# Optimization experiments

Hardware: AMD Instinct MI355X
Metric: run time of the kernel (lower is better)

The kernel has to match this reference:

```python
import jax, jax.numpy as jnp
import numpy as np

N_HASHES = 4
CHUNK = 144


def conv2d(x, w, b, pad):
    y = jax.lax.conv_general_dilated(x, w, (1, 1), [(pad, pad), (pad, pad)],
                                     dimension_numbers=('NCHW', 'OIHW', 'NCHW'))
    return y + b[None, :, None, None]


def resblock(x, w1, b1, w2, b2, ws=None, bs=None):
    # conv3x3 -> ReLU -> conv3x3 + skip (1x1 projection when channels change)
    h = conv2d(x, w1, b1, 1)
    h = jax.nn.relu(h)
    h = conv2d(h, w2, b2, 1)
    skip = x if ws is None else conv2d(x, ws, bs, 0)
    return skip + h


def _forward(feature_dec1, feature_dec2, reference_feature,
             mw1, mb1, mw2, mb2, mws, mbs,
             a1w1, a1b1, a1w2, a1b2, a2w1, a2b1, a2w2, a2b2,
             random_index):
    fd1 = jax.lax.stop_gradient(feature_dec1)  # is_detach=True default
    fd2 = jax.lax.stop_gradient(feature_dec2)
    B, C0, H, W = fd1.shape
    L = H * W
    # embeddings: (B, L, C) with C = C0 // reduction, and (B, L, C0) assemblies
    f1 = resblock(fd1, mw1, mb1, mw2, mb2, mws, mbs).reshape(B, -1, L).transpose(0, 2, 1)
    f2 = resblock(fd2, mw1, mb1, mw2, mb2, mws, mbs).reshape(B, -1, L).transpose(0, 2, 1)
    aux1 = resblock(fd1, a1w1, a1b1, a1w2, a1b2).reshape(B, -1, L).transpose(0, 2, 1)
    refe = resblock(reference_feature, a2w1, a2b1, a2w2, a2b2).reshape(B, -1, L).transpose(0, 2, 1)
    C = f1.shape[-1]
    inv_random_index = jnp.argsort(random_index)
    hb = min(2 * L // CHUNK + (2 * L // CHUNK) % 2, 128)
    f1f2 = jnp.concatenate([f1, f2], axis=1)            # (B, 2L, C)
    # LSH hashing (random rotations drawn with a fixed key, matching randn-per-call in torch)
    rot = jax.random.normal(jax.random.key(42), (C, N_HASHES, hb // 2), dtype=f1f2.dtype)
    rv = jnp.einsum('btf,fhi->bhti', f1f2, rot)
    rv = jnp.concatenate([rv, -rv], axis=-1)
    codes = jnp.argmax(rv, axis=-1)                     # (B, nh, 2L)
    codes = codes + (jnp.arange(N_HASHES) * hb)[None, :, None]
    codes = codes[:, :, random_index].reshape(B, -1)    # (B, nh*2L)
    indices = jnp.argsort(codes, axis=-1)
    undo_sort = jnp.argsort(indices, axis=-1)
    mod_indices = (indices % 2) * L                     # faithful to torch `indices % 2 * L` precedence
    zo = jnp.concatenate([jnp.full((B, L), 0.01, f1.dtype),
                          jnp.full((B, L), 0.99, f1.dtype)], axis=1)
    f1f2_p = f1f2[:, random_index, :]
    q = jnp.take_along_axis(f1f2_p, mod_indices[:, :, None], axis=1)
    zo_p = zo[:, random_index]
    z = jnp.take_along_axis(zo_p, mod_indices, axis=1)
    refw = jnp.concatenate([aux1, refe], axis=1)[:, random_index, :]
    r = jnp.take_along_axis(refw, mod_indices[:, :, None], axis=1)
    rem = (2 * L) % CHUNK
    padding = CHUNK - rem if rem != 0 else 0
    qb = q.reshape(B, N_HASHES, 2 * L, C)
    zb = z.reshape(B, N_HASHES, 2 * L)
    rb = r.reshape(B, N_HASHES, 2 * L, -1)
    if padding:
        qb = jnp.concatenate([qb, qb[:, :, -padding:]], axis=2)
        zb = jnp.concatenate([zb, zb[:, :, -padding:]], axis=2)
        rb = jnp.concatenate([rb, rb[:, :, -padding:]], axis=2)
    k = qb.shape[2] // CHUNK
    qb = qb.reshape(B, N_HASHES, k, CHUNK, C)
    zb = zb.reshape(B, N_HASHES, k, CHUNK)
    rb = rb.reshape(B, N_HASHES, k, CHUNK, -1)
    # F.normalize(p=2, dim=-1, eps=5e-5)
    norm = jnp.sqrt(jnp.sum(qb * qb, axis=-1, keepdims=True))
    km = qb / jnp.maximum(norm, 5e-5)
    adj = lambda x: jnp.concatenate([x, jnp.roll(x, 1, axis=2), jnp.roll(x, -1, axis=2)], axis=3)
    km, zb3, rb3 = adj(km), adj(zb), adj(rb)            # keys/vals over 3 adjacent buckets
    raw = jnp.einsum('bhkie,bhkje->bhkij', qb, km)      # (B,nh,k,144,432)
    w = jnp.exp(raw) * zb3[:, :, :, None, :]
    denom = jnp.sum(w, axis=-1, keepdims=True)
    score = w / denom
    bucket_score = denom.reshape(B, N_HASHES, -1)
    ret = jnp.einsum('bhkij,bhkje->bhkie', score, rb3)  # (B,nh,k,144,C0)
    CR = rb3.shape[-1]
    ret = ret.reshape(B, N_HASHES, -1, CR)
    if padding:
        ret = ret[:, :, :-padding]
        bucket_score = bucket_score[:, :, :-padding]
    ret = ret.reshape(B, N_HASHES * 2 * L, CR)
    bucket_score = bucket_score.reshape(B, -1)
    ret = jnp.take_along_axis(ret, undo_sort[:, :, None], axis=1)
    bucket_score = jnp.take_along_axis(bucket_score, undo_sort, axis=1)
    ret = ret.reshape(B, N_HASHES, 2 * L, CR)
    bucket_score = bucket_score.reshape(B, N_HASHES, 2 * L, 1)
    probs = bucket_score / jnp.sum(bucket_score, axis=1, keepdims=True)
    ret = jnp.sum(ret * probs, axis=1)                  # (B, 2L, CR)
    ret = ret.transpose(0, 2, 1)[:, :, inv_random_index]
    return ret.reshape(B, CR, 2, H, W)[:, :, 0]         # (B, C0, H, W)


def setup_inputs() -> dict:
    key = jax.random.key(0)
    ks = jax.random.split(key, 12)
    B, C0, H, W = 2, 64, 100, 100
    red = 4
    Cm = C0 // red
    s = jnp.float32(0.05)
    rn = lambda i, shape: jax.random.normal(ks[i], shape, dtype=jnp.float32)
    return {
        'feature_dec1': rn(0, (B, C0, H, W)),
        'feature_dec2': rn(1, (B, C0, H, W)),
        'reference_feature': rn(2, (B, C0, H, W)),
        'random_index': jax.random.permutation(ks[3], 2 * H * W).astype(jnp.int32),
        'mw1': rn(4, (Cm, C0, 3, 3)) * s, 'mb1': jnp.zeros((Cm,), jnp.float32),
        'mw2': rn(5, (Cm, Cm, 3, 3)) * s, 'mb2': jnp.zeros((Cm,), jnp.float32),
        'mws': rn(6, (Cm, C0, 1, 1)) * s, 'mbs': jnp.zeros((Cm,), jnp.float32),
        'a1w1': rn(7, (C0, C0, 3, 3)) * s, 'a1b1': jnp.zeros((C0,), jnp.float32),
        'a1w2': rn(8, (C0, C0, 3, 3)) * s, 'a1b2': jnp.zeros((C0,), jnp.float32),
        'a2w1': rn(9, (C0, C0, 3, 3)) * s, 'a2b1': jnp.zeros((C0,), jnp.float32),
        'a2w2': rn(10, (C0, C0, 3, 3)) * s, 'a2b2': jnp.zeros((C0,), jnp.float32),
    }


def reference(feature_dec1, feature_dec2, reference_feature, random_index,
              mw1, mb1, mw2, mb2, mws, mbs,
              a1w1, a1b1, a1w2, a1b2, a2w1, a2b1, a2w2, a2b2):
    return _forward(feature_dec1, feature_dec2, reference_feature,
                    mw1, mb1, mw2, mb2, mws, mbs,
                    a1w1, a1b1, a1w2, a1b2, a2w1, a2b1, a2w2, a2b2,
                    random_index)
```

## Files before the change

kernel.cpp:

```cpp
#include <hip/hip_runtime.h>

#define JAX_THREEFRY_PARTITIONABLE 1

namespace {

constexpr int BN   = 2;
constexpr int C0   = 64;
constexpr int HH   = 100;
constexpr int WWW  = 100;
constexpr int LL   = 10000;
constexpr int TL   = 20000;
constexpr int CHK  = 144;
constexpr int NCHK = 139;
constexpr int NPAD = 16;
constexpr int WINR = 432;

constexpr int OFF_ROT  = 0;
constexpr int OFF_WT1  = OFF_ROT + 4096;
constexpr int OFF_WT2  = OFF_WT1 + 9216;
constexpr int OFF_WTS  = OFF_WT2 + 2304;
constexpr int OFF_HT0  = OFF_WTS + 1024;
constexpr int OFF_HT1  = OFF_HT0 + 640000;
constexpr int OFF_HT2  = OFF_HT1 + 640000;
constexpr int OFF_HT3  = OFF_HT2 + 640000;
constexpr int OFF_F    = OFF_HT3 + 640000;
constexpr int OFF_SC   = OFF_F + 640000;
constexpr int OFF_CODE = OFF_SC + 272;
constexpr int OFF_RANK = OFF_CODE + 40000;
constexpr int OFF_N0   = OFF_RANK + 160000;
constexpr int OFF_INV  = OFF_N0 + 1112;
constexpr int OFF_AUX  = OFF_INV + 10000;

constexpr int AUXW = 36864;

__device__ __forceinline__ unsigned rotl32(unsigned v, int r) {
  return (v << r) | (v >> (32 - r));
}

__device__ void tf2x32(unsigned k0, unsigned k1, unsigned x0, unsigned x1,
                       unsigned& o0, unsigned& o1) {
  unsigned ks2 = k0 ^ k1 ^ 0x1BD11BDAu;
  x0 += k0; x1 += k1;
#define TFR(r) { x0 += x1; x1 = rotl32(x1, r); x1 ^= x0; }
  TFR(13) TFR(15) TFR(26) TFR(6)  x0 += k1;  x1 += ks2 + 1u;
  TFR(17) TFR(29) TFR(16) TFR(24) x0 += ks2; x1 += k0 + 2u;
  TFR(13) TFR(15) TFR(26) TFR(6)  x0 += k0;  x1 += k1 + 3u;
  TFR(17) TFR(29) TFR(16) TFR(24) x0 += k1;  x1 += ks2 + 4u;
  TFR(13) TFR(15) TFR(26) TFR(6)  x0 += ks2; x1 += k0 + 5u;
#undef TFR
  o0 = x0; o1 = x1;
}

__device__ float xla_erfinv(float x) {
#pragma clang fp contract(off)
  float w = -log1pf(-x * x);
  float p;
  if (w < 5.0f) {
    w = w - 2.5f;
    p = 2.81022636e-08f;
    p = 3.43273939e-07f  + p * w;
    p = -3.5233877e-06f  + p * w;
    p = -4.39150654e-06f + p * w;
    p = 0.00021858087f   + p * w;
    p = -0.00125372503f  + p * w;
    p = -0.00417768164f  + p * w;
    p = 0.246640727f     + p * w;
    p = 1.50140941f      + p * w;
  } else {
    w = sqrtf(w) - 3.0f;
    p = -0.000200214257f;
    p = 0.000100950558f + p * w;
    p = 0.00134934322f  + p * w;
    p = -0.00367342844f + p * w;
    p = 0.00573950773f  + p * w;
    p = -0.0076224613f  + p * w;
    p = 0.00943887047f  + p * w;
    p = 1.00167406f     + p * w;
    p = 2.83297682f     + p * w;
  }
  return p * x;
}

__global__ void k_prep(const float* __restrict__ mw1, const float* __restrict__ mw2,
                       const float* __restrict__ mws,
                       const float* __restrict__ a1w1, const float* __restrict__ a1w2,
                       const float* __restrict__ a2w1, const float* __restrict__ a2w2,
                       const int* __restrict__ ri,
                       float* __restrict__ rotT, float* __restrict__ wT1,
                       float* __restrict__ wT2, float* __restrict__ wTs,
                       float* __restrict__ auxT, int* __restrict__ inv) {
  int gid = blockIdx.x * 256 + threadIdx.x;
  if (gid < 4 * AUXW) {
    int wsel = gid / AUXW, j = gid % AUXW;
    const float* src = (wsel == 0) ? a1w1 : (wsel == 1) ? a1w2 : (wsel == 2) ? a2w1 : a2w2;
    int co = j / 576, r = j % 576;
    auxT[wsel * AUXW + r * 64 + co] = src[j];
    return;
  }
  int g2 = gid - 4 * AUXW;
  if (g2 < 4096) {
    int i = g2;
    unsigned o0, o1, bits;
#if JAX_THREEFRY_PARTITIONABLE
    tf2x32(0u, 42u, 0u, (unsigned)i, o0, o1);
    bits = o0 ^ o1;
#else
    if (i < 2048) { tf2x32(0u, 42u, (unsigned)i, (unsigned)(i + 2048), o0, o1); bits = o0; }
    else          { tf2x32(0u, 42u, (unsigned)(i - 2048), (unsigned)i, o0, o1); bits = o1; }
#endif
    unsigned fb = (bits >> 9) | 0x3f800000u;
    float f = __uint_as_float(fb) - 1.0f;
    const float lo = __uint_as_float(0xBF7FFFFFu);
    float u = fmaxf(lo, f * 2.0f + lo);
    float r = __uint_as_float(0x3FB504F3u) * xla_erfinv(u);
    int c = i >> 8, h = (i >> 6) & 3, j = i & 63;
    rotT[(h * 64 + j) * 16 + c] = r;
    return;
  }
  int g3 = g2 - 4096;
  if (g3 < 9216) {
    { int o = g3 / 576; int r = g3 % 576; wT1[r * 16 + o] = mw1[g3]; }
    if (g3 < 2304) { int o = g3 / 144; int r = g3 % 144; wT2[r * 16 + o] = mw2[g3]; }
    if (g3 < 1024) { int o = g3 / 64;  int ci = g3 % 64; wTs[ci * 16 + o] = mws[g3]; }
    return;
  }
  int g4 = g3 - 9216;
  if (g4 < TL) {
    int p = ri[g4];
    if (p < LL) inv[p] = g4;
  }
}

__global__ __launch_bounds__(256) void k_conv1(
    const float* __restrict__ fd1, const float* __restrict__ fd2,
    const float* __restrict__ wT1,
    float* __restrict__ ht0, float* __restrict__ ht1,
    float* __restrict__ ht2, float* __restrict__ ht3) {
  int x = blockIdx.x;
  int blk = (x & 7) * 98 + (x >> 3);
  int kq = blk & 3;
  int rest = blk >> 2;
  int n = rest / 49, tile = rest % 49;
  int ty0 = (tile / 7) * 16, tx0 = (tile % 7) * 16;
  const float* in = ((n >> 1) ? fd2 : fd1) + (n & 1) * (C0 * LL) + (kq * 16) * LL;
  float* htk = ((kq == 0) ? ht0 : (kq == 1) ? ht1 : (kq == 2) ? ht2 : ht3) + n * 16 * LL;
  int tid = threadIdx.x;
  int co = tid & 15, yl = tid >> 4;

  __shared__ float sIn[16 * 18 * 20];
  __shared__ float sW[144 * 16];

  for (int i = tid; i < 144 * 16; i += 256) sW[i] = wT1[kq * 2304 + i];
  for (int idx = tid; idx < 16 * 18 * 18; idx += 256) {
    int ci = idx / 324, r = idx % 324, iy = r / 18, ix = r % 18;
    int gy = ty0 - 1 + iy, gx = tx0 - 1 + ix;
    float v = 0.f;
    if (gy >= 0 && gy < HH && gx >= 0 && gx < WWW) v = in[ci * LL + gy * WWW + gx];
    sIn[ci * 360 + iy * 20 + ix] = v;
  }
  __syncthreads();

  float acc[16];
#pragma unroll
  for (int p = 0; p < 16; ++p) acc[p] = 0.f;

  for (int cc = 0; cc < 4; ++cc) {
    float w[4][9];
#pragma unroll
    for (int c4 = 0; c4 < 4; ++c4)
#pragma unroll
      for (int t = 0; t < 9; ++t)
        w[c4][t] = sW[((cc * 4 + c4) * 9 + t) * 16 + co];
#pragma unroll
    for (int c4 = 0; c4 < 4; ++c4) {
      const float* rowb = &sIn[(cc * 4 + c4) * 360 + yl * 20];
#pragma unroll
      for (int dy = 0; dy < 3; ++dy) {
        const float* r = rowb + dy * 20;
        float v[18];
#pragma unroll
        for (int k = 0; k < 18; ++k) v[k] = r[k];
#pragma unroll
        for (int dx = 0; dx < 3; ++dx) {
          float wv = w[c4][dy * 3 + dx];
#pragma unroll
          for (int p = 0; p < 16; ++p) acc[p] = fmaf(v[p + dx], wv, acc[p]);
        }
      }
    }
  }

  int yv = ty0 + yl;
  if (yv < HH) {
    float* op = htk + co * LL + yv * WWW;
#pragma unroll
    for (int g = 0; g < 4; ++g) {
      int xg = tx0 + g * 4;
      if (xg < WWW) {
        float4 s = make_float4(acc[g * 4], acc[g * 4 + 1], acc[g * 4 + 2], acc[g * 4 + 3]);
        *(float4*)&op[xg] = s;
      }
    }
  }
}

__global__ __launch_bounds__(512) void k_conv2(
    const float* __restrict__ fd1, const float* __restrict__ fd2,
    const float* __restrict__ ht0, const float* __restrict__ ht1,
    const float* __restrict__ ht2, const float* __restrict__ ht3,
    const float* __restrict__ wT2, const float* __restrict__ mb1,
    const float* __restrict__ mb2, const float* __restrict__ wTs,
    const float* __restrict__ mbs, float* __restrict__ F) {
  int xx = blockIdx.x;
  int xcd = xx & 7, slot = xx >> 3;
  int blk = (xcd < 4) ? (xcd * 46 + slot) : (184 + (xcd - 4) * 45 + slot);
  int n = blk / 91, tile = blk % 91;
  int yt = tile / 7, xt = tile % 7;
  int ty0 = yt * 8, tx0 = xt * 16;
  int src = n >> 1, b = n & 1;
  const float* in = (src ? fd2 : fd1) + b * (C0 * LL);
  const float* h0 = ht0 + n * 16 * LL;
  const float* h1 = ht1 + n * 16 * LL;
  const float* h2 = ht2 + n * 16 * LL;
  const float* h3 = ht3 + n * 16 * LL;
  int tid = threadIdx.x;
  int co = tid & 15, xq = (tid >> 4) & 3, yl = tid >> 6;

  __shared__ float sW2[144 * 16];
  __shared__ float sWs[64 * 16];
  __shared__ float sH[16 * 10 * 20];
  __shared__ float sSkip[16 * 8 * 17];

  for (int i = tid; i < 144 * 16; i += 512) sW2[i] = wT2[i];
  for (int i = tid; i < 64 * 16; i += 512) sWs[i] = wTs[i];
  for (int idx = tid; idx < 16 * 10 * 18; idx += 512) {
    int ci = idx / 180, r = idx % 180, iy = r / 18, ix = r % 18;
    int gy = ty0 - 1 + iy, gx = tx0 - 1 + ix;
    float v = 0.f;
    if (gy >= 0 && gy < HH && gx >= 0 && gx < WWW) {
      int o = ci * LL + gy * WWW + gx;
      v = fmaxf(h0[o] + h1[o] + h2[o] + h3[o] + mb1[ci], 0.f);
    }
    sH[ci * 200 + iy * 20 + ix] = v;
  }
  __syncthreads();

  float acc[4];
  float bias = mb2[co] + mbs[co];
#pragma unroll
  for (int p = 0; p < 4; ++p) acc[p] = bias;

  for (int ci = 0; ci < 16; ++ci) {
    const float* rowb = &sH[ci * 200 + yl * 20 + xq * 4];
#pragma unroll
    for (int dy = 0; dy < 3; ++dy) {
      const float* r = rowb + dy * 20;
      float v[6];
#pragma unroll
      for (int k = 0; k < 6; ++k) v[k] = r[k];
#pragma unroll
      for (int dx = 0; dx < 3; ++dx) {
        float wv = sW2[(ci * 9 + dy * 3 + dx) * 16 + co];
#pragma unroll
        for (int p = 0; p < 4; ++p) acc[p] = fmaf(v[p + dx], wv, acc[p]);
      }
    }
  }

  for (int cc = 0; cc < 4; ++cc) {
    __syncthreads();
    for (int idx = tid; idx < 16 * 8 * 16; idx += 512) {
      int ci = idx >> 7, r = idx & 127, iy = r >> 4, ix = r & 15;
      int gy = ty0 + iy, gx = tx0 + ix;
      float v = 0.f;
      if (gy < HH && gx < WWW) v = in[(cc * 16 + ci) * LL + gy * WWW + gx];
      sSkip[(ci * 8 + iy) * 17 + ix] = v;
    }
    __syncthreads();
    for (int c16 = 0; c16 < 16; ++c16) {
      float wv = sWs[(cc * 16 + c16) * 16 + co];
      const float* sv = &sSkip[(c16 * 8 + yl) * 17 + xq * 4];
#pragma unroll
      for (int p = 0; p < 4; ++p) acc[p] = fmaf(sv[p], wv, acc[p]);
    }
  }

  int yv = ty0 + yl;
  if (yv < HH) {
    float* Fb = F + (b * TL + src * LL + yv * WWW) * 16 + co;
#pragma unroll
    for (int p = 0; p < 4; ++p) {
      int xv = tx0 + xq * 4 + p;
      if (xv < WWW) Fb[xv * 16] = acc[p];
    }
  }
}

__global__ __launch_bounds__(256) void k_codes(
    const float* __restrict__ F, const float* __restrict__ rotT,
    const int* __restrict__ ri, unsigned char* __restrict__ codes) {
  int bh = blockIdx.y;
  int b = bh >> 2, h = bh & 3;
  __shared__ float srot[1024];
  int tid = threadIdx.x;
  for (int i = tid; i < 1024; i += 256) srot[i] = rotT[h * 1024 + i];
  __syncthreads();
  int t = blockIdx.x * 256 + tid;
  if (t >= TL) return;
  int pos = ri[t];
  const float* Fr = F + (b * TL + pos) * 16;
  float q[16];
#pragma unroll
  for (int c = 0; c < 16; ++c) q[c] = Fr[c];
  float best = -1e30f; int bi = 0;
  float worst = 1e30f; int wi = 0;
  for (int j = 0; j < 64; ++j) {
    float v = 0.f;
    const float* rp = srot + j * 16;
#pragma unroll
    for (int c = 0; c < 16; ++c) v = fmaf(q[c], rp[c], v);
    if (v > best)  { best = v;  bi = j; }
    if (v < worst) { worst = v; wi = j; }
  }
  int code = (best >= -worst) ? bi : (64 + wi);
  codes[bh * TL + t] = (unsigned char)code;
}

__global__ __launch_bounds__(256) void k_sort(
    const unsigned char* __restrict__ codes,
    int* __restrict__ rank_of, int* __restrict__ n0g) {
  int bh = blockIdx.x;
  const unsigned char* keys = codes + bh * TL;
  __shared__ unsigned short cnt[240][128];
  __shared__ unsigned int totals[128];
  __shared__ unsigned int baseoff[128];
  __shared__ unsigned int n0s[NCHK];
  int tid = threadIdx.x;
  for (int i = tid; i < 240 * 128 / 2; i += 256) ((unsigned int*)cnt)[i] = 0u;
  for (int i = tid; i < NCHK; i += 256) n0s[i] = 0u;
  __syncthreads();
  const int SEG = 84;
  int base = tid * SEG;
  int nloc = (tid < 240) ? (TL - base) : 0;
  if (nloc > SEG) nloc = SEG;
  if (nloc < 0) nloc = 0;
  for (int e = 0; e < nloc; ++e) cnt[tid][keys[base + e]]++;
  __syncthreads();
  if (tid < 128) {
    unsigned int s = 0;
    for (int g = 0; g < 240; ++g) s += cnt[g][tid];
    totals[tid] = s;
  }
  __syncthreads();
  if (tid == 0) {
    unsigned int run = 0;
    for (int c = 0; c < 128; ++c) { baseoff[c] = run; run += totals[c]; }
  }
  __syncthreads();
  if (tid < 128) {
    unsigned int run = baseoff[tid];
    for (int g = 0; g < 240; ++g) {
      unsigned int v = cnt[g][tid];
      cnt[g][tid] = (unsigned short)run;
      run += v;
    }
  }
  __syncthreads();
  for (int e = 0; e < nloc; ++e) {
    int idx = base + e;
    int c = keys[idx];
    int r = cnt[tid][c]++;
    rank_of[bh * TL + idx] = r;
    if (!(idx & 1)) {
      atomicAdd(&n0s[r / CHK], 1u);
      if (r >= TL - NPAD) atomicAdd(&n0s[NCHK - 1], 1u);
    }
  }
  __syncthreads();
  for (int i = tid; i < NCHK; i += 256) n0g[bh * NCHK + i] = (int)n0s[i];
}

__global__ __launch_bounds__(576) void k_point(
    const float* __restrict__ fd1, const float* __restrict__ refin,
    const int* __restrict__ ri, const float* __restrict__ auxT,
    const float* __restrict__ a1b1, const float* __restrict__ a1b2,
    const float* __restrict__ a2b1, const float* __restrict__ a2b2,
    const float* __restrict__ F, float* __restrict__ SC) {
  int tid = threadIdx.x;
  if (blockIdx.x == 4) {
#pragma clang fp contract(off)
    int b = tid;
    if (b >= BN) return;
    int j0 = ri[0], jL = ri[LL];
    const float* qA = F + (b * TL + j0) * 16;
    const float* qB = F + (b * TL + jL) * 16;
    float nA = 0.f, nB = 0.f;
    for (int c = 0; c < 16; ++c) { nA += qA[c] * qA[c]; nB += qB[c] * qB[c]; }
    float mA = fmaxf(sqrtf(nA), 5e-5f), mB = fmaxf(sqrtf(nB), 5e-5f);
    float d00 = 0.f, d01 = 0.f, d10 = 0.f, d11 = 0.f;
    for (int c = 0; c < 16; ++c) {
      float kAc = qA[c] / mA, kBc = qB[c] / mB;
      d00 += qA[c] * kAc; d01 += qA[c] * kBc;
      d10 += qB[c] * kAc; d11 += qB[c] * kBc;
    }
    float zA = (j0 < LL) ? 0.01f : 0.99f;
    float zB = (jL < LL) ? 0.01f : 0.99f;
    float* sc = SC + b * 136;
    sc[0] = expf(d00) * zA; sc[1] = expf(d01) * zB;
    sc[2] = expf(d10) * zA; sc[3] = expf(d11) * zB;
    return;
  }
  int b = blockIdx.x & 1, which = blockIdx.x >> 1;
  int pos = ri[which * LL];
  const float *in, *w1T, *b1, *w2T, *b2;
  int sp;
  if (pos < LL) {
    in = fd1 + b * C0 * LL; w1T = auxT; b1 = a1b1; w2T = auxT + AUXW; b2 = a1b2; sp = pos;
  } else {
    in = refin + b * C0 * LL; w1T = auxT + 2 * AUXW; b1 = a2b1; w2T = auxT + 3 * AUXW;
    b2 = a2b2; sp = pos - LL;
  }
  int y = sp / WWW, x = sp % WWW;

  __shared__ float sPatch[64][25];
  __shared__ float sW[144 * 64];
  __shared__ float sH[9][64];
  __shared__ float sPart[9][64];

  for (int idx = tid; idx < 64 * 25; idx += 576) {
    int ci = idx / 25, pp = idx % 25;
    int gy = y - 2 + pp / 5, gx = x - 2 + pp % 5;
    float v = 0.f;
    if (gy >= 0 && gy < HH && gx >= 0 && gx < WWW) v = in[ci * LL + gy * WWW + gx];
    sPatch[ci][pp] = v;
  }

  int p = tid / 64, ch = tid & 63;
  int p3 = p / 3, pm = p % 3;
  int yy = y + p3 - 1, xx = x + pm - 1;
  bool inb = (yy >= 0) && (yy < HH) && (xx >= 0) && (xx < WWW);

  float acc0 = 0.f, acc1 = 0.f;
  for (int cc = 0; cc < 4; ++cc) {
    __syncthreads();
    for (int i = tid; i < 144 * 64; i += 576) sW[i] = w1T[cc * 9216 + i];
    __syncthreads();
    if (inb) {
#pragma unroll
      for (int ci = 0; ci < 16; ++ci) {
        const float* wp = &sW[ci * 9 * 64 + ch];
        const float* pr = &sPatch[cc * 16 + ci][0];
#pragma unroll
        for (int t = 0; t < 9; ++t) {
          float v = pr[(p3 + t / 3) * 5 + (pm + t % 3)];
          if (ci & 1) acc1 = fmaf(v, wp[t * 64], acc1);
          else        acc0 = fmaf(v, wp[t * 64], acc0);
        }
      }
    }
  }
  sH[p][ch] = inb ? fmaxf(acc0 + acc1 + b1[ch], 0.f) : 0.f;
  __syncthreads();

  {
    float part = 0.f;
    const float* wbase = w2T + p * 64 + ch;
    for (int ci = 0; ci < 64; ++ci) part = fmaf(sH[p][ci], wbase[ci * 9 * 64], part);
    sPart[p][ch] = part;
  }
  __syncthreads();
  if (tid < 64) {
    int co = tid;
    float a = in[co * LL + y * WWW + x] + b2[co];
#pragma unroll
    for (int g = 0; g < 9; ++g) a += sPart[g][co];
    SC[b * 136 + 4 + which * 64 + co] = a;
  }
}

__global__ __launch_bounds__(256) void k_out(
    const int* __restrict__ inv, const int* __restrict__ rank_of,
    const int* __restrict__ n0, const float* __restrict__ SC,
    float* __restrict__ out) {
  int b = blockIdx.y;
  int p = blockIdx.x * 256 + threadIdx.x;
  if (p >= LL) return;
  int t = inv[p];
  int si = t & 1;
  float e0 = SC[b * 136 + si * 2 + 0];
  float e1 = SC[b * 136 + si * 2 + 1];
  float s0 = 0.f, s1 = 0.f;
  for (int h = 0; h < 4; ++h) {
    int r = rank_of[(b * 4 + h) * TL + t];
    int k = r / CHK;
    int km = (k == 0) ? NCHK - 1 : k - 1;
    int kp = (k == NCHK - 1) ? 0 : k + 1;
    const int* nb = n0 + (b * 4 + h) * NCHK;
    int W0 = nb[k] + nb[km] + nb[kp];
    s0 += (float)W0 * e0;
    s1 += (float)(WINR - W0) * e1;
  }
  float invd = 1.f / (s0 + s1);
  float al = s0 * invd;
  float be = s1 * invd;
  const float* rA = SC + b * 136 + 4;
  const float* rB = rA + 64;
  float* o = out + b * C0 * LL + p;
#pragma unroll
  for (int c = 0; c < 64; ++c) o[c * LL] = al * rA[c] + be * rB[c];
}

}

extern "C" void kernel_launch(void* const* d_in, const int* in_sizes, int n_in,
                              void* d_out, int out_size, void* d_ws, size_t ws_size,
                              hipStream_t stream) {
  const float* fd1  = (const float*)d_in[0];
  const float* fd2  = (const float*)d_in[1];
  const float* reff = (const float*)d_in[2];
  const int*   ri   = (const int*)d_in[3];
  const float* mw1  = (const float*)d_in[4];
  const float* mb1  = (const float*)d_in[5];
  const float* mw2  = (const float*)d_in[6];
  const float* mb2  = (const float*)d_in[7];
  const float* mws  = (const float*)d_in[8];
  const float* mbs  = (const float*)d_in[9];
  const float* a1w1 = (const float*)d_in[10];
  const float* a1b1 = (const float*)d_in[11];
  const float* a1w2 = (const float*)d_in[12];
  const float* a1b2 = (const float*)d_in[13];
  const float* a2w1 = (const float*)d_in[14];
  const float* a2b1 = (const float*)d_in[15];
  const float* a2w2 = (const float*)d_in[16];
  const float* a2b2 = (const float*)d_in[17];

  float* ws = (float*)d_ws;
  float* rotT = ws + OFF_ROT;
  float* wT1  = ws + OFF_WT1;
  float* wT2  = ws + OFF_WT2;
  float* wTs  = ws + OFF_WTS;
  float* ht0  = ws + OFF_HT0;
  float* ht1  = ws + OFF_HT1;
  float* ht2  = ws + OFF_HT2;
  float* ht3  = ws + OFF_HT3;
  float* F    = ws + OFF_F;
  float* SC   = ws + OFF_SC;
  unsigned char* codes = (unsigned char*)(ws + OFF_CODE);
  int* rank_of = (int*)(ws + OFF_RANK);
  int* n0      = (int*)(ws + OFF_N0);
  int* invp    = (int*)(ws + OFF_INV);
  float* auxT  = ws + OFF_AUX;

  k_prep<<<dim3(707), dim3(256), 0, stream>>>(mw1, mw2, mws, a1w1, a1w2, a2w1, a2w2,
                                              ri, rotT, wT1, wT2, wTs, auxT, invp);
  k_conv1<<<dim3(784), dim3(256), 0, stream>>>(fd1, fd2, wT1, ht0, ht1, ht2, ht3);
  k_conv2<<<dim3(364), dim3(512), 0, stream>>>(fd1, fd2, ht0, ht1, ht2, ht3, wT2,
                                               mb1, mb2, wTs, mbs, F);
  k_codes<<<dim3(79, 8), dim3(256), 0, stream>>>(F, rotT, ri, codes);
  k_sort<<<dim3(8), dim3(256), 0, stream>>>(codes, rank_of, n0);
  k_point<<<dim3(5), dim3(576), 0, stream>>>(fd1, reff, ri, auxT, a1b1, a1b2,
                                             a2b1, a2b2, F, SC);
  k_out<<<dim3(40, 2), dim3(256), 0, stream>>>(invp, rank_of, n0, SC, (float*)d_out);
}
```

Measured before the change: 132.8 us.

## Shrink conv1 tiles, fuse codes with point kernel, split output by channel

conv1 now uses 8-row tiles with 512 threads and 4 outputs per thread, giving more blocks and fewer registers per thread. The LSH code computation and the aux point evaluation are merged into one launch, which removes a kernel launch and lets the small point blocks overlap with hashing. k_out gains a z-dimension splitting its 64 output channels into 4 groups for more parallelism. Smaller conv tiles raise halo overhead and reload weights more often.

```diff
diff --git a/kernel.cpp b/kernel.cpp
--- a/kernel.cpp
+++ b/kernel.cpp
@@ -131,38 +131,39 @@
   }
 }
 
-__global__ __launch_bounds__(256) void k_conv1(
+__global__ __launch_bounds__(512) void k_conv1(
     const float* __restrict__ fd1, const float* __restrict__ fd2,
     const float* __restrict__ wT1,
     float* __restrict__ ht0, float* __restrict__ ht1,
     float* __restrict__ ht2, float* __restrict__ ht3) {
   int x = blockIdx.x;
-  int blk = (x & 7) * 98 + (x >> 3);
+  int blk = (x & 7) * 182 + (x >> 3);
   int kq = blk & 3;
   int rest = blk >> 2;
-  int n = rest / 49, tile = rest % 49;
-  int ty0 = (tile / 7) * 16, tx0 = (tile % 7) * 16;
+  int n = rest / 91, tile = rest % 91;
+  int yt = tile / 7, xt = tile % 7;
+  int ty0 = yt * 8, tx0 = xt * 16;
   const float* in = ((n >> 1) ? fd2 : fd1) + (n & 1) * (C0 * LL) + (kq * 16) * LL;
   float* htk = ((kq == 0) ? ht0 : (kq == 1) ? ht1 : (kq == 2) ? ht2 : ht3) + n * 16 * LL;
   int tid = threadIdx.x;
-  int co = tid & 15, yl = tid >> 4;
-
-  __shared__ float sIn[16 * 18 * 20];
+  int co = tid & 15, xq = (tid >> 4) & 3, yl = tid >> 6;
+
+  __shared__ float sIn[16 * 10 * 20];
   __shared__ float sW[144 * 16];
 
-  for (int i = tid; i < 144 * 16; i += 256) sW[i] = wT1[kq * 2304 + i];
-  for (int idx = tid; idx < 16 * 18 * 18; idx += 256) {
-    int ci = idx / 324, r = idx % 324, iy = r / 18, ix = r % 18;
+  for (int i = tid; i < 144 * 16; i += 512) sW[i] = wT1[kq * 2304 + i];
+  for (int idx = tid; idx < 16 * 10 * 18; idx += 512) {
+    int ci = idx / 180, r = idx % 180, iy = r / 18, ix = r % 18;
     int gy = ty0 - 1 + iy, gx = tx0 - 1 + ix;
     float v = 0.f;
     if (gy >= 0 && gy < HH && gx >= 0 && gx < WWW) v = in[ci * LL + gy * WWW + gx];
-    sIn[ci * 360 + iy * 20 + ix] = v;
-  }
-  __syncthreads();
-
-  float acc[16];
-#pragma unroll
-  for (int p = 0; p < 16; ++p) acc[p] = 0.f;
+    sIn[ci * 200 + iy * 20 + ix] = v;
+  }
+  __syncthreads();
+
+  float acc[4];
+#pragma unroll
+  for (int p = 0; p < 4; ++p) acc[p] = 0.f;
 
   for (int cc = 0; cc < 4; ++cc) {
     float w[4][9];
@@ -173,34 +174,28 @@
         w[c4][t] = sW[((cc * 4 + c4) * 9 + t) * 16 + co];
 #pragma unroll
     for (int c4 = 0; c4 < 4; ++c4) {
-      const float* rowb = &sIn[(cc * 4 + c4) * 360 + yl * 20];
+      const float* rowb = &sIn[(cc * 4 + c4) * 200 + yl * 20 + xq * 4];
 #pragma unroll
       for (int dy = 0; dy < 3; ++dy) {
         const float* r = rowb + dy * 20;
-        float v[18];
-#pragma unroll
-        for (int k = 0; k < 18; ++k) v[k] = r[k];
+        float v[6];
+#pragma unroll
+        for (int k = 0; k < 6; ++k) v[k] = r[k];
 #pragma unroll
         for (int dx = 0; dx < 3; ++dx) {
           float wv = w[c4][dy * 3 + dx];
 #pragma unroll
-          for (int p = 0; p < 16; ++p) acc[p] = fmaf(v[p + dx], wv, acc[p]);
+          for (int p = 0; p < 4; ++p) acc[p] = fmaf(v[p + dx], wv, acc[p]);
         }
       }
     }
   }
 
   int yv = ty0 + yl;
-  if (yv < HH) {
-    float* op = htk + co * LL + yv * WWW;
-#pragma unroll
-    for (int g = 0; g < 4; ++g) {
-      int xg = tx0 + g * 4;
-      if (xg < WWW) {
-        float4 s = make_float4(acc[g * 4], acc[g * 4 + 1], acc[g * 4 + 2], acc[g * 4 + 3]);
-        *(float4*)&op[xg] = s;
-      }
-    }
+  int xg = tx0 + xq * 4;
+  if (yv < HH && xg < WWW) {
+    float4 s = make_float4(acc[0], acc[1], acc[2], acc[3]);
+    *(float4*)&htk[co * LL + yv * WWW + xg] = s;
   }
 }
 
@@ -296,98 +291,46 @@
   }
 }
 
-__global__ __launch_bounds__(256) void k_codes(
+__global__ __launch_bounds__(576) void k_codes(
     const float* __restrict__ F, const float* __restrict__ rotT,
-    const int* __restrict__ ri, unsigned char* __restrict__ codes) {
-  int bh = blockIdx.y;
-  int b = bh >> 2, h = bh & 3;
-  __shared__ float srot[1024];
-  int tid = threadIdx.x;
-  for (int i = tid; i < 1024; i += 256) srot[i] = rotT[h * 1024 + i];
-  __syncthreads();
-  int t = blockIdx.x * 256 + tid;
-  if (t >= TL) return;
-  int pos = ri[t];
-  const float* Fr = F + (b * TL + pos) * 16;
-  float q[16];
-#pragma unroll
-  for (int c = 0; c < 16; ++c) q[c] = Fr[c];
-  float best = -1e30f; int bi = 0;
-  float worst = 1e30f; int wi = 0;
-  for (int j = 0; j < 64; ++j) {
-    float v = 0.f;
-    const float* rp = srot + j * 16;
-#pragma unroll
-    for (int c = 0; c < 16; ++c) v = fmaf(q[c], rp[c], v);
-    if (v > best)  { best = v;  bi = j; }
-    if (v < worst) { worst = v; wi = j; }
-  }
-  int code = (best >= -worst) ? bi : (64 + wi);
-  codes[bh * TL + t] = (unsigned char)code;
-}
-
-__global__ __launch_bounds__(256) void k_sort(
-    const unsigned char* __restrict__ codes,
-    int* __restrict__ rank_of, int* __restrict__ n0g) {
-  int bh = blockIdx.x;
-  const unsigned char* keys = codes + bh * TL;
-  __shared__ unsigned short cnt[240][128];
-  __shared__ unsigned int totals[128];
-  __shared__ unsigned int baseoff[128];
-  __shared__ unsigned int n0s[NCHK];
-  int tid = threadIdx.x;
-  for (int i = tid; i < 240 * 128 / 2; i += 256) ((unsigned int*)cnt)[i] = 0u;
-  for (int i = tid; i < NCHK; i += 256) n0s[i] = 0u;
-  __syncthreads();
-  const int SEG = 84;
-  int base = tid * SEG;
-  int nloc = (tid < 240) ? (TL - base) : 0;
-  if (nloc > SEG) nloc = SEG;
-  if (nloc < 0) nloc = 0;
-  for (int e = 0; e < nloc; ++e) cnt[tid][keys[base + e]]++;
-  __syncthreads();
-  if (tid < 128) {
-    unsigned int s = 0;
-    for (int g = 0; g < 240; ++g) s += cnt[g][tid];
-    totals[tid] = s;
-  }
-  __syncthreads();
-  if (tid == 0) {
-    unsigned int run = 0;
-    for (int c = 0; c < 128; ++c) { baseoff[c] = run; run += totals[c]; }
-  }
-  __syncthreads();
-  if (tid < 128) {
-    unsigned int run = baseoff[tid];
-    for (int g = 0; g < 240; ++g) {
-      unsigned int v = cnt[g][tid];
-      cnt[g][tid] = (unsigned short)run;
-      run += v;
-    }
-  }
-  __syncthreads();
-  for (int e = 0; e < nloc; ++e) {
-    int idx = base + e;
-    int c = keys[idx];
-    int r = cnt[tid][c]++;
-    rank_of[bh * TL + idx] = r;
-    if (!(idx & 1)) {
-      atomicAdd(&n0s[r / CHK], 1u);
-      if (r >= TL - NPAD) atomicAdd(&n0s[NCHK - 1], 1u);
-    }
-  }
-  __syncthreads();
-  for (int i = tid; i < NCHK; i += 256) n0g[bh * NCHK + i] = (int)n0s[i];
-}
-
-__global__ __launch_bounds__(576) void k_point(
+    const int* __restrict__ ri, unsigned char* __restrict__ codes,
     const float* __restrict__ fd1, const float* __restrict__ refin,
-    const int* __restrict__ ri, const float* __restrict__ auxT,
+    const float* __restrict__ auxT,
     const float* __restrict__ a1b1, const float* __restrict__ a1b2,
     const float* __restrict__ a2b1, const float* __restrict__ a2b2,
-    const float* __restrict__ F, float* __restrict__ SC) {
+    float* __restrict__ SC) {
+  int blk = blockIdx.x;
   int tid = threadIdx.x;
-  if (blockIdx.x == 4) {
+
+  if (blk < 280) {
+    int bh = blk / 35, seg = blk % 35;
+    int b = bh >> 2, h = bh & 3;
+    __shared__ float srot[1024];
+    for (int i = tid; i < 1024; i += 576) srot[i] = rotT[h * 1024 + i];
+    __syncthreads();
+    int t = seg * 576 + tid;
+    if (t >= TL) return;
+    int pos = ri[t];
+    const float* Fr = F + (b * TL + pos) * 16;
+    float q[16];
+#pragma unroll
+    for (int c = 0; c < 16; ++c) q[c] = Fr[c];
+    float best = -1e30f; int bi = 0;
+    float worst = 1e30f; int wi = 0;
+    for (int j = 0; j < 64; ++j) {
+      float v = 0.f;
+      const float* rp = srot + j * 16;
+#pragma unroll
+      for (int c = 0; c < 16; ++c) v = fmaf(q[c], rp[c], v);
+      if (v > best)  { best = v;  bi = j; }
+      if (v < worst) { worst = v; wi = j; }
+    }
+    int code = (best >= -worst) ? bi : (64 + wi);
+    codes[bh * TL + t] = (unsigned char)code;
+    return;
+  }
+
+  if (blk == 284) {
 #pragma clang fp contract(off)
     int b = tid;
     if (b >= BN) return;
@@ -410,7 +353,9 @@
     sc[2] = expf(d10) * zA; sc[3] = expf(d11) * zB;
     return;
   }
-  int b = blockIdx.x & 1, which = blockIdx.x >> 1;
+
+  int pb = blk - 280;
+  int b = pb & 1, which = pb >> 1;
   int pos = ri[which * LL];
   const float *in, *w1T, *b1, *w2T, *b2;
   int sp;
@@ -478,11 +423,66 @@
   }
 }
 
+__global__ __launch_bounds__(256) void k_sort(
+    const unsigned char* __restrict__ codes,
+    int* __restrict__ rank_of, int* __restrict__ n0g) {
+  int bh = blockIdx.x;
+  const unsigned char* keys = codes + bh * TL;
+  __shared__ unsigned short cnt[240][128];
+  __shared__ unsigned int totals[128];
+  __shared__ unsigned int baseoff[128];
+  __shared__ unsigned int n0s[NCHK];
+  int tid = threadIdx.x;
+  for (int i = tid; i < 240 * 128 / 2; i += 256) ((unsigned int*)cnt)[i] = 0u;
+  for (int i = tid; i < NCHK; i += 256) n0s[i] = 0u;
+  __syncthreads();
+  const int SEG = 84;
+  int base = tid * SEG;
+  int nloc = (tid < 240) ? (TL - base) : 0;
+  if (nloc > SEG) nloc = SEG;
+  if (nloc < 0) nloc = 0;
+  for (int e = 0; e < nloc; ++e) cnt[tid][keys[base + e]]++;
+  __syncthreads();
+  if (tid < 128) {
+    unsigned int s = 0;
+    for (int g = 0; g < 240; ++g) s += cnt[g][tid];
+    totals[tid] = s;
+  }
+  __syncthreads();
+  if (tid == 0) {
+    unsigned int run = 0;
+    for (int c = 0; c < 128; ++c) { baseoff[c] = run; run += totals[c]; }
+  }
+  __syncthreads();
+  if (tid < 128) {
+    unsigned int run = baseoff[tid];
+    for (int g = 0; g < 240; ++g) {
+      unsigned int v = cnt[g][tid];
+      cnt[g][tid] = (unsigned short)run;
+      run += v;
+    }
+  }
+  __syncthreads();
+  for (int e = 0; e < nloc; ++e) {
+    int idx = base + e;
+    int c = keys[idx];
+    int r = cnt[tid][c]++;
+    rank_of[bh * TL + idx] = r;
+    if (!(idx & 1)) {
+      atomicAdd(&n0s[r / CHK], 1u);
+      if (r >= TL - NPAD) atomicAdd(&n0s[NCHK - 1], 1u);
+    }
+  }
+  __syncthreads();
+  for (int i = tid; i < NCHK; i += 256) n0g[bh * NCHK + i] = (int)n0s[i];
+}
+
 __global__ __launch_bounds__(256) void k_out(
     const int* __restrict__ inv, const int* __restrict__ rank_of,
     const int* __restrict__ n0, const float* __restrict__ SC,
     float* __restrict__ out) {
   int b = blockIdx.y;
+  int c0 = blockIdx.z * 16;
   int p = blockIdx.x * 256 + threadIdx.x;
   if (p >= LL) return;
   int t = inv[p];
@@ -507,7 +507,7 @@
   const float* rB = rA + 64;
   float* o = out + b * C0 * LL + p;
 #pragma unroll
-  for (int c = 0; c < 64; ++c) o[c * LL] = al * rA[c] + be * rB[c];
+  for (int c = 0; c < 16; ++c) o[(c0 + c) * LL] = al * rA[c0 + c] + be * rB[c0 + c];
 }
 
 }
@@ -553,12 +553,11 @@
 
   k_prep<<<dim3(707), dim3(256), 0, stream>>>(mw1, mw2, mws, a1w1, a1w2, a2w1, a2w2,
                                               ri, rotT, wT1, wT2, wTs, auxT, invp);
-  k_conv1<<<dim3(784), dim3(256), 0, stream>>>(fd1, fd2, wT1, ht0, ht1, ht2, ht3);
+  k_conv1<<<dim3(1456), dim3(512), 0, stream>>>(fd1, fd2, wT1, ht0, ht1, ht2, ht3);
   k_conv2<<<dim3(364), dim3(512), 0, stream>>>(fd1, fd2, ht0, ht1, ht2, ht3, wT2,
                                                mb1, mb2, wTs, mbs, F);
-  k_codes<<<dim3(79, 8), dim3(256), 0, stream>>>(F, rotT, ri, codes);
+  k_codes<<<dim3(285), dim3(576), 0, stream>>>(F, rotT, ri, codes, fd1, reff, auxT,
+                                               a1b1, a1b2, a2b1, a2b2, SC);
   k_sort<<<dim3(8), dim3(256), 0, stream>>>(codes, rank_of, n0);
-  k_point<<<dim3(5), dim3(576), 0, stream>>>(fd1, reff, ri, auxT, a1b1, a1b2,
-                                             a2b1, a2b2, F, SC);
-  k_out<<<dim3(40, 2), dim3(256), 0, stream>>>(invp, rank_of, n0, SC, (float*)d_out);
-}
+  k_out<<<dim3(40, 2, 4), dim3(256), 0, stream>>>(invp, rank_of, n0, SC, (float*)d_out);
+}
```

Measured after the change: 126.7 us. -4.6%, faster.
